# Performance work log

Measured on AMD Instinct MI355X. Metric: run time of the kernel, lower is better.

The kernel has to match this reference:

```python
import jax, jax.numpy as jnp
import numpy as np

KMAX = 16
NEG_INF = -1e9


def setup_inputs() -> dict:
    key = jax.random.key(0)
    ks = jax.random.split(key, 8)
    B, N, H = 65536, 512, 256
    L = KMAX + 1
    actions = jax.random.randint(ks[0], (B, L), 0, N + 1)  # values in [0, N], N == STOP
    rp = jax.random.uniform(ks[1], (B, 1), dtype=jnp.float32)
    s1 = 1.0 / np.sqrt(N + 3)
    s2 = 1.0 / np.sqrt(H)
    W1 = jax.random.normal(ks[2], (N + 3, H), dtype=jnp.float32) * s1
    b1 = jax.random.normal(ks[3], (H,), dtype=jnp.float32) * 0.01
    W2 = jax.random.normal(ks[4], (H, H), dtype=jnp.float32) * s2
    b2 = jax.random.normal(ks[5], (H,), dtype=jnp.float32) * 0.01
    Wh = jax.random.normal(ks[6], (H, N + 1), dtype=jnp.float32) * s2
    bh = jax.random.normal(ks[7], (N + 1,), dtype=jnp.float32) * 0.01
    return {"actions": actions, "rp": rp, "W1": W1, "b1": b1, "W2": W2, "b2": b2, "Wh": Wh, "bh": bh}


def reference(actions, rp, W1, b1, W2, b2, Wh, bh):
    B, L = actions.shape
    N = Wh.shape[1] - 1
    f32 = rp.dtype

    def step_fn(carry, a):
        sel_mask, k_sel, step, logpf = carry  # [B,N], [B,1], [B,1], [B]
        x = jnp.concatenate([sel_mask, k_sel, step, rp], axis=-1)  # [B, N+3]
        h = jax.nn.relu(x @ W1 + b1)
        h = jax.nn.relu(h @ W2 + b2)
        logits = h @ Wh + bh  # [B, N+1]
        k = k_sel[:, 0]
        full = (k >= KMAX).astype(f32)[:, None]
        mask_assets = (1.0 - sel_mask) * (1.0 - full)  # cannot re-add or exceed Kmax
        mask_stop = (k > 0).astype(f32)[:, None]       # cannot STOP on empty set
        mask = jnp.concatenate([mask_assets, mask_stop], axis=-1)
        logits = jnp.where(mask <= 0.0, NEG_INF, logits)
        logp = jax.nn.log_softmax(logits, axis=-1)
        alive = a >= 0
        a_safe = jnp.clip(a, 0, N)
        chosen = jnp.take_along_axis(logp, a_safe[:, None], axis=-1)[:, 0]
        logpf = logpf + jnp.where(alive, chosen, 0.0)
        stop = (a == N) & alive
        add = (alive & (~stop)).astype(f32)[:, None]
        # one_hot of N/-1 is all-zero, so only valid adds update sel_mask
        upd = jax.nn.one_hot(a_safe, N, dtype=f32) * add
        sel_mask = jnp.maximum(sel_mask, upd)
        k_sel = jnp.sum(sel_mask, axis=-1, keepdims=True)
        step = step + 1.0
        return (sel_mask, k_sel, step, logpf), None

    init = (jnp.zeros((B, N), f32), jnp.zeros((B, 1), f32), jnp.zeros((B, 1), f32), jnp.zeros((B,), f32))
    (_, _, _, logpf), _ = jax.lax.scan(step_fn, init, actions.T)  # scan over L steps
    return logpf
```

## Files before the change

kernel.cpp:

```cpp
#include <hip/hip_runtime.h>


#define NEG_INF (-1000000000.0f)
#define LOG2E 1.4426950408889634f
#define LN2   0.6931471805599453f

#define A_NEW  0x400

#define HST 1040
#define HKT 2080

typedef short bf16x8 __attribute__((ext_vector_type(8)));
typedef float f32x16 __attribute__((ext_vector_type(16)));

__device__ __forceinline__ unsigned short f2bf(float x){
  unsigned int u = __float_as_uint(x);
  u = (u + 0x7FFFu + ((u >> 16) & 1u)) >> 16;
  return (unsigned short)u;
}
__device__ __forceinline__ float bf2f(unsigned short h){
  return __uint_as_float(((unsigned int)h) << 16);
}
__device__ __forceinline__ unsigned int cvt_pk_bf16(float lo, float hi){
  unsigned int r;
  asm("v_cvt_pk_bf16_f32 %0, %1, %2" : "=v"(r) : "v"(lo), "v"(hi));
  return r;
}
__device__ __forceinline__ float4 ld4bf(const unsigned short* p){
  ushort4 u = *(const ushort4*)p;
  return make_float4(bf2f(u.x), bf2f(u.y), bf2f(u.z), bf2f(u.w));
}

__global__ void prep_kernel(const float* __restrict__ W2, const float* __restrict__ Wh,
                            unsigned short* __restrict__ w2f, unsigned short* __restrict__ whf,
                            float* __restrict__ whstop){
  int id = blockIdx.x * 256 + threadIdx.x;
  if (id < 8192){
    int lane = id & 63; int tile = id >> 6;
    int ntg = tile & 7, kt = tile >> 3;
    int col = ntg * 32 + (lane & 31);
    int k0  = kt * 16 + (lane >> 5) * 8;
    unsigned int u[4];
#pragma unroll
    for (int p = 0; p < 4; ++p){
      unsigned short lo = f2bf(W2[(k0 + 2*p    ) * 256 + col]);
      unsigned short hi = f2bf(W2[(k0 + 2*p + 1) * 256 + col]);
      u[p] = (unsigned int)lo | ((unsigned int)hi << 16);
    }
    *(uint4*)(w2f + (size_t)id * 8) = make_uint4(u[0], u[1], u[2], u[3]);
  } else if (id < 24576){
    int id2 = id - 8192;
    int lane = id2 & 63; int tile = id2 >> 6;
    int ntg = tile & 15, kt = tile >> 4;
    int col = ntg * 32 + (lane & 31);
    int k0  = kt * 16 + (lane >> 5) * 8;
    unsigned int u[4];
#pragma unroll
    for (int p = 0; p < 4; ++p){
      unsigned short lo = f2bf(Wh[(k0 + 2*p    ) * 513 + col] * LOG2E);
      unsigned short hi = f2bf(Wh[(k0 + 2*p + 1) * 513 + col] * LOG2E);
      u[p] = (unsigned int)lo | ((unsigned int)hi << 16);
    }
    *(uint4*)(whf + (size_t)id2 * 8) = make_uint4(u[0], u[1], u[2], u[3]);
  } else if (id < 24832){
    int k = id - 24576;
    whstop[k] = Wh[k * 513 + 512];
  }
}

__launch_bounds__(256, 4)
__global__ void gfn_kernel(const int* __restrict__ actions, const float* __restrict__ rp,
                           const float* __restrict__ W1, const float* __restrict__ b1,
                           const float* __restrict__ b2, const float* __restrict__ bh,
                           const unsigned short* __restrict__ w2f,
                           const unsigned short* __restrict__ whf,
                           const float* __restrict__ whstop,
                           float* __restrict__ out)
{
  __shared__ alignas(16) char h[32 * HST];
  __shared__ alignas(16) unsigned short c16[1024];
  __shared__ alignas(16) unsigned short bhl216[512];
  __shared__ alignas(16) unsigned short b2s16[256];
  __shared__ alignas(16) unsigned short whst_h[256];
  __shared__ alignas(16) unsigned short amask[18][32];
  __shared__ alignas(16) float pred[64][4];
  __shared__ alignas(16) float stopp[64];
  __shared__ alignas(16) float chosen[64];

  const int tid  = threadIdx.x;
  const int wave = tid >> 6;
  const int lane = tid & 63;
  const int ln5  = lane & 31;
  const int lg2  = lane >> 5;
  const int base = blockIdx.x * 32;

  for (int i = tid; i < 1024; i += 256){
    int rrow = i >> 8, f = i & 255;
    float v = (rrow < 3) ? W1[(512 + rrow) * 256 + f] : b1[f];
    c16[i] = f2bf(v);
  }
  b2s16[tid] = f2bf(b2[tid]);
  whst_h[tid] = f2bf(whstop[tid]);
  for (int i = tid; i < 512; i += 256){
    int pt = i >> 5, l2 = (i >> 4) & 1, r = i & 15;
    int col = pt * 32 + (r & 3) + 8 * (r >> 2) + 4 * l2;
    bhl216[i] = f2bf(bh[col] * LOG2E);
  }
  const float stopbias = bh[512];
  if (tid < 64) stopp[tid] = 0.f;
  int* acts = (int*)h;
  for (int i = tid; i < 544; i += 256) acts[i] = actions[base * 17 + i];
  float logpf = 0.f;
  uint4 selw_r = make_uint4(0u, 0u, 0u, 0u);
  __syncthreads();

  if (tid < 32){
    int s = tid, k = 0;
    for (int t = 0; t < 17; ++t){
      int a = acts[s * 17 + t];
      bool alive = (a >= 0);
      bool isnew = alive && (a < 512);
      if (isnew){
        for (int u = 0; u < t; ++u) if (acts[s * 17 + u] == a){ isnew = false; break; }
      }
      int av = alive ? a : 1023;
      amask[t][s] = (unsigned short)(av | (isnew ? A_NEW : 0) | (k << 11));
      if (isnew) ++k;
    }
    amask[17][s] = (unsigned short)(1023 | (k << 11));
  }
  unsigned int Spk[16];
#pragma unroll
  for (int j = 0; j < 16; ++j) Spk[j] = 0u;
  __syncthreads();

  const int aw_base = (lane >> 1) * HST + (lane & 1) * 8 + wave * 128;
  const int br_base = lg2 * HST;
  const int bw_base = wave * 8 * HST + lg2 * 8;
  const int cr_base = lg2 * HST + ln5 * 16;
  const int rpu = __builtin_amdgcn_readfirstlane(base + wave * 8);

#pragma unroll 1
  for (int c = 0; c < 9; ++c){
    const int t = c * 2;

    {
      const float4 ck4 = ld4bf(&c16[lane * 4]);
      const float4 ct4 = ld4bf(&c16[256 + lane * 4]);
      const float4 cr4 = ld4bf(&c16[512 + lane * 4]);
      const float4 cb4 = ld4bf(&c16[768 + lane * 4]);
      float tf = (float)t;
      float c00 = cb4.x + tf * ct4.x, c01 = cb4.y + tf * ct4.y;
      float c02 = cb4.z + tf * ct4.z, c03 = cb4.w + tf * ct4.w;
#pragma unroll
      for (int s8 = 0; s8 < 8; ++s8){
        int s = wave * 8 + s8;
        float rv = rp[rpu + s8];
        int m0 = amask[t][s];
        int m1 = amask[t + 1][s];
        unsigned int pk0 = Spk[s8 * 2], pk1 = Spk[s8 * 2 + 1];
        float S0 = __uint_as_float(pk0 << 16);
        float S1 = __uint_as_float(pk0 & 0xFFFF0000u);
        float S2 = __uint_as_float(pk1 << 16);
        float S3 = __uint_as_float(pk1 & 0xFFFF0000u);
        float kf = (float)(m0 >> 11);
        float v0 = S0 + kf * ck4.x + rv * cr4.x + c00;
        float v1 = S1 + kf * ck4.y + rv * cr4.y + c01;
        float v2 = S2 + kf * ck4.z + rv * cr4.z + c02;
        float v3 = S3 + kf * ck4.w + rv * cr4.w + c03;
        *(uint2*)(h + aw_base + s8 * 16) =
            make_uint2(cvt_pk_bf16(fmaxf(v0,0.f), fmaxf(v1,0.f)),
                       cvt_pk_bf16(fmaxf(v2,0.f), fmaxf(v3,0.f)));
        float d0 = ct4.x, d1 = ct4.y, d2 = ct4.z, d3 = ct4.w;
        if (m0 & A_NEW){
          int a = m0 & 1023;
          float4 w = *(const float4*)(W1 + (size_t)a * 256 + lane * 4);
          S0 += w.x; S1 += w.y; S2 += w.z; S3 += w.w;
          d0 += w.x + ck4.x; d1 += w.y + ck4.y; d2 += w.z + ck4.z; d3 += w.w + ck4.w;
        }
        v0 += d0; v1 += d1; v2 += d2; v3 += d3;
        *(uint2*)(h + aw_base + 512 + s8 * 16) =
            make_uint2(cvt_pk_bf16(fmaxf(v0,0.f), fmaxf(v1,0.f)),
                       cvt_pk_bf16(fmaxf(v2,0.f), fmaxf(v3,0.f)));
        if (m1 & A_NEW){
          int a = m1 & 1023;
          float4 w = *(const float4*)(W1 + (size_t)a * 256 + lane * 4);
          S0 += w.x; S1 += w.y; S2 += w.z; S3 += w.w;
        }
        if ((m0 | m1) & A_NEW){
          Spk[s8 * 2]     = cvt_pk_bf16(S0, S1);
          Spk[s8 * 2 + 1] = cvt_pk_bf16(S2, S3);
        }
      }
    }
    __syncthreads();

#pragma unroll 1
    for (int q = 0; q < 2; ++q){
      const int rr = q * 32 + ln5;
      const int brq = br_base + rr * 16;
      f32x16 aB0, aB1;
#pragma unroll
      for (int i = 0; i < 16; ++i){ aB0[i] = 0.f; aB1[i] = 0.f; }
#pragma unroll 4
      for (int kt = 0; kt < 16; ++kt){
        bf16x8 sf = *(const bf16x8*)(h + brq + kt * HKT);
        bf16x8 w0 = *(const bf16x8*)(w2f + ((size_t)((kt * 8 + wave * 2    ) * 64 + lane)) * 8);
        bf16x8 w1 = *(const bf16x8*)(w2f + ((size_t)((kt * 8 + wave * 2 + 1) * 64 + lane)) * 8);
        aB0 = __builtin_amdgcn_mfma_f32_32x32x16_bf16(w0, sf, aB0, 0, 0, 0);
        aB1 = __builtin_amdgcn_mfma_f32_32x32x16_bf16(w1, sf, aB1, 0, 0, 0);
      }
      __syncthreads();
      const int bwq = bw_base + rr * 16;
      float sp = 0.f;
#pragma unroll
      for (int g = 0; g < 4; ++g){
        int f0 = wave * 64 + g * 8 + lg2 * 4;
        int f1 = f0 + 32;
        float4 bb0 = ld4bf(&b2s16[f0]);
        float4 bb1 = ld4bf(&b2s16[f1]);
        float4 ws0 = ld4bf(&whst_h[f0]);
        float4 ws1 = ld4bf(&whst_h[f1]);
        {
          float v0 = fmaxf(aB0[g*4+0] + bb0.x, 0.f), v1 = fmaxf(aB0[g*4+1] + bb0.y, 0.f);
          float v2 = fmaxf(aB0[g*4+2] + bb0.z, 0.f), v3 = fmaxf(aB0[g*4+3] + bb0.w, 0.f);
          sp += v0 * ws0.x + v1 * ws0.y + v2 * ws0.z + v3 * ws0.w;
          *(uint2*)(h + bwq + g * HST) = make_uint2(cvt_pk_bf16(v0, v1), cvt_pk_bf16(v2, v3));
        }
        {
          float v0 = fmaxf(aB1[g*4+0] + bb1.x, 0.f), v1 = fmaxf(aB1[g*4+1] + bb1.y, 0.f);
          float v2 = fmaxf(aB1[g*4+2] + bb1.z, 0.f), v3 = fmaxf(aB1[g*4+3] + bb1.w, 0.f);
          sp += v0 * ws1.x + v1 * ws1.y + v2 * ws1.z + v3 * ws1.w;
          *(uint2*)(h + bwq + (g + 4) * HST) = make_uint2(cvt_pk_bf16(v0, v1), cvt_pk_bf16(v2, v3));
        }
      }
      sp += __shfl_xor(sp, 32);
      if (lg2 == 0) atomicAdd(&stopp[rr], sp);
    }
    __syncthreads();

    {
      int mt  = amask[t][ln5];
      int mt1 = amask[t + 1][ln5];
      int av0 = mt & 1023, av1 = mt1 & 1023;
      int pa = (mt & A_NEW) ? av0 : -1;
      float sum0 = 0.f, sum1 = 0.f;
#pragma unroll 1
      for (int p = 0; p < 4; ++p){
        int pt = wave * 4 + p;
        const unsigned short* bi = &bhl216[pt * 32 + lg2 * 16];
        float4 b0_ = ld4bf(bi);
        float4 b1_ = ld4bf(bi + 4);
        float4 b2_ = ld4bf(bi + 8);
        float4 b3_ = ld4bf(bi + 12);
        f32x16 a0, a1;
        a0[0]=b0_.x; a0[1]=b0_.y; a0[2]=b0_.z; a0[3]=b0_.w;
        a0[4]=b1_.x; a0[5]=b1_.y; a0[6]=b1_.z; a0[7]=b1_.w;
        a0[8]=b2_.x; a0[9]=b2_.y; a0[10]=b2_.z; a0[11]=b2_.w;
        a0[12]=b3_.x; a0[13]=b3_.y; a0[14]=b3_.z; a0[15]=b3_.w;
        a1 = a0;
#pragma unroll 4
        for (int kt = 0; kt < 16; ++kt){
          bf16x8 f0 = *(const bf16x8*)(h + cr_base + kt * HKT);
          bf16x8 f1 = *(const bf16x8*)(h + cr_base + 512 + kt * HKT);
          bf16x8 w = *(const bf16x8*)(whf + ((size_t)((kt * 16 + pt) * 64 + lane)) * 8);
          a0 = __builtin_amdgcn_mfma_f32_32x32x16_bf16(w, f0, a0, 0, 0, 0);
          a1 = __builtin_amdgcn_mfma_f32_32x32x16_bf16(w, f1, a1, 0, 0, 0);
        }
        unsigned wlo = (p & 1) ? selw_r.y : selw_r.x;
        unsigned whi = (p & 1) ? selw_r.w : selw_r.z;
        unsigned word = (p & 2) ? whi : wlo;
        unsigned wsel = (word >> (lg2 * 16)) & 0xFFFFu;
        unsigned msk0 = (mt  & 0x8000) ? 0xFFFFu : wsel;
        unsigned msk1 = (mt1 & 0x8000) ? 0xFFFFu : wsel;
        if (pa >= 0 && (pa >> 5) == pt && (((pa >> 2) & 1) == lg2))
          msk1 |= 1u << ((pa & 3) | (((pa >> 3) & 3) << 2));
        int tr0 = (av0 < 512 && (av0 >> 5) == pt && (((av0 >> 2) & 1) == lg2))
                  ? ((av0 & 3) | (((av0 >> 3) & 3) << 2)) : -1;
        int tr1 = (av1 < 512 && (av1 >> 5) == pt && (((av1 >> 2) & 1) == lg2))
                  ? ((av1 & 3) | (((av1 >> 3) & 3) << 2)) : -1;
        float cv0 = 0.f, cv1 = 0.f;
#pragma unroll
        for (int r = 0; r < 16; ++r){
          float v0 = ((msk0 >> r) & 1u) ? NEG_INF : a0[r];
          float v1 = ((msk1 >> r) & 1u) ? NEG_INF : a1[r];
          sum0 += __builtin_amdgcn_exp2f(v0);
          sum1 += __builtin_amdgcn_exp2f(v1);
          if (r == tr0) cv0 = a0[r];
          if (r == tr1) cv1 = a1[r];
        }
        if (tr0 >= 0) chosen[ln5]      = cv0;
        if (tr1 >= 0) chosen[32 + ln5] = cv1;
      }
      sum0 += __shfl_xor(sum0, 32);
      sum1 += __shfl_xor(sum1, 32);
      if (lg2 == 0){
        pred[ln5][wave]      = sum0;
        pred[32 + ln5][wave] = sum1;
      }
#pragma unroll
      for (int e = 0; e < 2; ++e){
        int m = e ? mt1 : mt;
        if ((m & A_NEW) && (((m & 1023) >> 7) == wave)){
          int av = m & 1023;
          int w2 = (av >> 5) & 3;
          unsigned bit = 1u << ((((av >> 2) & 1) << 4) | (av & 3) | (((av >> 3) & 3) << 2));
          if (w2 == 0) selw_r.x |= bit;
          else if (w2 == 1) selw_r.y |= bit;
          else if (w2 == 2) selw_r.z |= bit;
          else selw_r.w |= bit;
        }
      }
    }
    __syncthreads();

    if (tid < 32){
      int s = tid;
      int m0 = amask[t][s];
      int m1 = amask[t + 1][s];
      int av0 = m0 & 1023, av1 = m1 & 1023;
      int k0 = m0 >> 11, k1 = m1 >> 11;
      float stop0 = (k0 == 0) ? NEG_INF : stopp[s] + stopbias;
      float stop1 = (k1 == 0) ? NEG_INF : stopp[32 + s] + stopbias;
      {
        float tot = __expf(stop0)
                  + pred[s][0] + pred[s][1] + pred[s][2] + pred[s][3];
        float lse = __logf(tot);
        if (av0 != 1023){
          float ch;
          if (av0 == 512) ch = stop0;
          else {
            bool mskd = !(m0 & A_NEW) || (k0 >= 16);
            ch = mskd ? NEG_INF : chosen[s] * LN2;
          }
          logpf += ch - lse;
        }
      }
      {
        int row = 32 + s;
        float tot = __expf(stop1)
                  + pred[row][0] + pred[row][1] + pred[row][2] + pred[row][3];
        float lse = __logf(tot);
        if (av1 != 1023){
          float ch;
          if (av1 == 512) ch = stop1;
          else {
            bool mskd = !(m1 & A_NEW) || (k1 >= 16);
            ch = mskd ? NEG_INF : chosen[row] * LN2;
          }
          logpf += ch - lse;
        }
      }
      stopp[s] = 0.f; stopp[32 + s] = 0.f;
    }
    __syncthreads();
  }

  if (tid < 32) out[base + tid] = logpf;
}

extern "C" void kernel_launch(void* const* d_in, const int* in_sizes, int n_in,
                              void* d_out, int out_size, void* d_ws, size_t ws_size,
                              hipStream_t stream)
{
  const int*   actions = (const int*)d_in[0];
  const float* rp  = (const float*)d_in[1];
  const float* W1  = (const float*)d_in[2];
  const float* b1  = (const float*)d_in[3];
  const float* W2  = (const float*)d_in[4];
  const float* b2  = (const float*)d_in[5];
  const float* Wh  = (const float*)d_in[6];
  const float* bh  = (const float*)d_in[7];
  float* out = (float*)d_out;

  unsigned short* w2f = (unsigned short*)d_ws;
  unsigned short* whf = w2f + 65536;
  float* whstop = (float*)(whf + 131072);

  prep_kernel<<<97, 256, 0, stream>>>(W2, Wh, w2f, whf, whstop);
  gfn_kernel<<<2048, 256, 0, stream>>>(actions, rp, W1, b1, b2, bh, w2f, whf, whstop, out);
}
```

Baseline: 618.6 us.

## Reorder weight fragment layout, keep biases in fp32, accumulate softmax sums atomically

Pre-packed W2 and Wh fragments are reordered so each wave's column tile is contiguous across kt, and the inner loops now use per-wave base pointers with constant strides instead of recomputed index arithmetic. Biases move from bf16 to fp32 in LDS, which avoids unpacking. Per-wave softmax partial sums are accumulated with LDS atomics into one predsum array rather than a [64][4] table, and the chosen logit is stored as bf16. The atomics add contention and the bf16 chosen value loses precision in the log-probability.

```diff
diff --git a/kernel.cpp b/kernel.cpp
--- a/kernel.cpp
+++ b/kernel.cpp
@@ -37,7 +37,7 @@
   int id = blockIdx.x * 256 + threadIdx.x;
   if (id < 8192){
     int lane = id & 63; int tile = id >> 6;
-    int ntg = tile & 7, kt = tile >> 3;
+    int ntg = tile >> 4, kt = tile & 15;
     int col = ntg * 32 + (lane & 31);
     int k0  = kt * 16 + (lane >> 5) * 8;
     unsigned int u[4];
@@ -51,8 +51,8 @@
   } else if (id < 24576){
     int id2 = id - 8192;
     int lane = id2 & 63; int tile = id2 >> 6;
-    int ntg = tile & 15, kt = tile >> 4;
-    int col = ntg * 32 + (lane & 31);
+    int pt = tile >> 4, kt = tile & 15;
+    int col = pt * 32 + (lane & 31);
     int k0  = kt * 16 + (lane >> 5) * 8;
     unsigned int u[4];
 #pragma unroll
@@ -79,13 +79,13 @@
 {
   __shared__ alignas(16) char h[32 * HST];
   __shared__ alignas(16) unsigned short c16[1024];
-  __shared__ alignas(16) unsigned short bhl216[512];
-  __shared__ alignas(16) unsigned short b2s16[256];
+  __shared__ alignas(16) float bhl2[512];
+  __shared__ alignas(16) float b2s[256];
   __shared__ alignas(16) unsigned short whst_h[256];
   __shared__ alignas(16) unsigned short amask[18][32];
-  __shared__ alignas(16) float pred[64][4];
+  __shared__ alignas(16) float predsum[64];
   __shared__ alignas(16) float stopp[64];
-  __shared__ alignas(16) float chosen[64];
+  __shared__ alignas(16) unsigned short chosen16[64];
 
   const int tid  = threadIdx.x;
   const int wave = tid >> 6;
@@ -99,15 +99,15 @@
     float v = (rrow < 3) ? W1[(512 + rrow) * 256 + f] : b1[f];
     c16[i] = f2bf(v);
   }
-  b2s16[tid] = f2bf(b2[tid]);
+  b2s[tid] = b2[tid];
   whst_h[tid] = f2bf(whstop[tid]);
   for (int i = tid; i < 512; i += 256){
     int pt = i >> 5, l2 = (i >> 4) & 1, r = i & 15;
     int col = pt * 32 + (r & 3) + 8 * (r >> 2) + 4 * l2;
-    bhl216[i] = f2bf(bh[col] * LOG2E);
+    bhl2[i] = bh[col] * LOG2E;
   }
   const float stopbias = bh[512];
-  if (tid < 64) stopp[tid] = 0.f;
+  if (tid < 64){ stopp[tid] = 0.f; predsum[tid] = 0.f; }
   int* acts = (int*)h;
   for (int i = tid; i < 544; i += 256) acts[i] = actions[base * 17 + i];
   float logpf = 0.f;
@@ -139,6 +139,9 @@
   const int bw_base = wave * 8 * HST + lg2 * 8;
   const int cr_base = lg2 * HST + ln5 * 16;
   const int rpu = __builtin_amdgcn_readfirstlane(base + wave * 8);
+  const unsigned lane8 = (unsigned)lane * 8u;
+  const unsigned short* w2p0 = w2f + (unsigned)(wave * 2    ) * 8192u + lane8;
+  const unsigned short* w2p1 = w2f + (unsigned)(wave * 2 + 1) * 8192u + lane8;
 
 #pragma unroll 1
   for (int c = 0; c < 9; ++c){
@@ -205,8 +208,8 @@
 #pragma unroll 4
       for (int kt = 0; kt < 16; ++kt){
         bf16x8 sf = *(const bf16x8*)(h + brq + kt * HKT);
-        bf16x8 w0 = *(const bf16x8*)(w2f + ((size_t)((kt * 8 + wave * 2    ) * 64 + lane)) * 8);
-        bf16x8 w1 = *(const bf16x8*)(w2f + ((size_t)((kt * 8 + wave * 2 + 1) * 64 + lane)) * 8);
+        bf16x8 w0 = *(const bf16x8*)(w2p0 + (unsigned)(kt * 512));
+        bf16x8 w1 = *(const bf16x8*)(w2p1 + (unsigned)(kt * 512));
         aB0 = __builtin_amdgcn_mfma_f32_32x32x16_bf16(w0, sf, aB0, 0, 0, 0);
         aB1 = __builtin_amdgcn_mfma_f32_32x32x16_bf16(w1, sf, aB1, 0, 0, 0);
       }
@@ -217,8 +220,8 @@
       for (int g = 0; g < 4; ++g){
         int f0 = wave * 64 + g * 8 + lg2 * 4;
         int f1 = f0 + 32;
-        float4 bb0 = ld4bf(&b2s16[f0]);
-        float4 bb1 = ld4bf(&b2s16[f1]);
+        float4 bb0 = *(const float4*)&b2s[f0];
+        float4 bb1 = *(const float4*)&b2s[f1];
         float4 ws0 = ld4bf(&whst_h[f0]);
         float4 ws1 = ld4bf(&whst_h[f1]);
         {
@@ -248,11 +251,12 @@
 #pragma unroll 1
       for (int p = 0; p < 4; ++p){
         int pt = wave * 4 + p;
-        const unsigned short* bi = &bhl216[pt * 32 + lg2 * 16];
-        float4 b0_ = ld4bf(bi);
-        float4 b1_ = ld4bf(bi + 4);
-        float4 b2_ = ld4bf(bi + 8);
-        float4 b3_ = ld4bf(bi + 12);
+        const unsigned short* wp = whf + (unsigned)pt * 8192u + lane8;
+        const float* bi = &bhl2[pt * 32 + lg2 * 16];
+        float4 b0_ = *(const float4*)(bi);
+        float4 b1_ = *(const float4*)(bi + 4);
+        float4 b2_ = *(const float4*)(bi + 8);
+        float4 b3_ = *(const float4*)(bi + 12);
         f32x16 a0, a1;
         a0[0]=b0_.x; a0[1]=b0_.y; a0[2]=b0_.z; a0[3]=b0_.w;
         a0[4]=b1_.x; a0[5]=b1_.y; a0[6]=b1_.z; a0[7]=b1_.w;
@@ -263,7 +267,7 @@
         for (int kt = 0; kt < 16; ++kt){
           bf16x8 f0 = *(const bf16x8*)(h + cr_base + kt * HKT);
           bf16x8 f1 = *(const bf16x8*)(h + cr_base + 512 + kt * HKT);
-          bf16x8 w = *(const bf16x8*)(whf + ((size_t)((kt * 16 + pt) * 64 + lane)) * 8);
+          bf16x8 w = *(const bf16x8*)(wp + (unsigned)(kt * 512));
           a0 = __builtin_amdgcn_mfma_f32_32x32x16_bf16(w, f0, a0, 0, 0, 0);
           a1 = __builtin_amdgcn_mfma_f32_32x32x16_bf16(w, f1, a1, 0, 0, 0);
         }
@@ -289,14 +293,14 @@
           if (r == tr0) cv0 = a0[r];
           if (r == tr1) cv1 = a1[r];
         }
-        if (tr0 >= 0) chosen[ln5]      = cv0;
-        if (tr1 >= 0) chosen[32 + ln5] = cv1;
+        if (tr0 >= 0) chosen16[ln5]      = f2bf(cv0);
+        if (tr1 >= 0) chosen16[32 + ln5] = f2bf(cv1);
       }
       sum0 += __shfl_xor(sum0, 32);
       sum1 += __shfl_xor(sum1, 32);
       if (lg2 == 0){
-        pred[ln5][wave]      = sum0;
-        pred[32 + ln5][wave] = sum1;
+        atomicAdd(&predsum[ln5], sum0);
+        atomicAdd(&predsum[32 + ln5], sum1);
       }
 #pragma unroll
       for (int e = 0; e < 2; ++e){
@@ -323,35 +327,33 @@
       float stop0 = (k0 == 0) ? NEG_INF : stopp[s] + stopbias;
       float stop1 = (k1 == 0) ? NEG_INF : stopp[32 + s] + stopbias;
       {
-        float tot = __expf(stop0)
-                  + pred[s][0] + pred[s][1] + pred[s][2] + pred[s][3];
+        float tot = __expf(stop0) + predsum[s];
         float lse = __logf(tot);
         if (av0 != 1023){
           float ch;
           if (av0 == 512) ch = stop0;
           else {
             bool mskd = !(m0 & A_NEW) || (k0 >= 16);
-            ch = mskd ? NEG_INF : chosen[s] * LN2;
+            ch = mskd ? NEG_INF : bf2f(chosen16[s]) * LN2;
           }
           logpf += ch - lse;
         }
       }
       {
-        int row = 32 + s;
-        float tot = __expf(stop1)
-                  + pred[row][0] + pred[row][1] + pred[row][2] + pred[row][3];
+        float tot = __expf(stop1) + predsum[32 + s];
         float lse = __logf(tot);
         if (av1 != 1023){
           float ch;
           if (av1 == 512) ch = stop1;
           else {
             bool mskd = !(m1 & A_NEW) || (k1 >= 16);
-            ch = mskd ? NEG_INF : chosen[row] * LN2;
+            ch = mskd ? NEG_INF : bf2f(chosen16[32 + s]) * LN2;
           }
           logpf += ch - lse;
         }
       }
       stopp[s] = 0.f; stopp[32 + s] = 0.f;
+      predsum[s] = 0.f; predsum[32 + s] = 0.f;
     }
     __syncthreads();
   }
```

After: 575.4 us. 1.08x faster.
